# Kernel optimization log

Measured on AMD Instinct MI355X. Metric: run time of the kernel, lower is better.

Reference implementation:

```python
import jax, jax.numpy as jnp
import numpy as np

B, M, E, H, TOPK = 1024, 10000, 8, 512, 2


def setup_inputs() -> dict:
    key = jax.random.key(0)
    ks = jax.random.split(key, 6)
    s_in = 1.0 / np.sqrt(M)
    s_h = 1.0 / np.sqrt(H)
    x = jax.random.normal(ks[0], (B, M), dtype=jnp.float32)
    # Expert params, torch Linear layout stacked over experts
    W1 = jax.random.uniform(ks[1], (E, H, M), jnp.float32, -s_in, s_in)
    b1 = jax.random.uniform(ks[2], (E, H), jnp.float32, -s_in, s_in)
    W2 = jax.random.uniform(ks[3], (E, M, H), jnp.float32, -s_h, s_h)
    b2 = jax.random.uniform(ks[4], (E, M), jnp.float32, -s_h, s_h)
    Wr = jax.random.uniform(ks[5], (E, M), jnp.float32, -s_in, s_in)  # router, no bias
    return {"x": x, "W1": W1, "b1": b1, "W2": W2, "b2": b2, "Wr": Wr}


def reference(x, W1, b1, W2, b2, Wr):
    # Router: logits [B, E], sparse top-k softmax weights scattered to dense [B, E]
    logits = jnp.einsum('bm,em->be', x, Wr)
    topk_vals, topk_idx = jax.lax.top_k(logits, TOPK)
    probs = jax.nn.softmax(topk_vals, axis=-1)
    rw = jnp.zeros_like(logits).at[jnp.arange(B)[:, None], topk_idx].set(probs)
    # Dense all-expert MLP (faithful to original: every expert runs on every token)
    h = jax.nn.relu(jnp.einsum('bm,ehm->beh', x, W1) + b1)      # [B, E, H]
    eo = jnp.einsum('beh,emh->bem', h, W2) + b2                  # [B, E, M]
    # Masked weighted combine
    out = jnp.sum(rw[:, :, None] * eo, axis=1)                   # [B, M]
    return out
```

## Files before the change

### kernel.cpp

```cpp
#include <hip/hip_runtime.h>
#include <hip/hip_bf16.h>


#define B_TOK 1024
#define M_DIM 10000
#define E_NUM 8
#define H_DIM 512
#define NSTEP 313
#define SPAD1 316

typedef __attribute__((ext_vector_type(4))) float fx4;
typedef __attribute__((ext_vector_type(8))) short sx8;
typedef __attribute__((ext_vector_type(4))) short sx4;

__device__ __forceinline__ short f2bf(float f) {
  union { __hip_bfloat16 h; short s; } u;
  u.h = __float2bfloat16(f);
  return u.s;
}

__device__ __forceinline__ sx8 pack8(fx4 a, fx4 b) {
  sx8 r;
  r[0] = f2bf(a[0]); r[1] = f2bf(a[1]); r[2] = f2bf(a[2]); r[3] = f2bf(a[3]);
  r[4] = f2bf(b[0]); r[5] = f2bf(b[1]); r[6] = f2bf(b[2]); r[7] = f2bf(b[3]);
  return r;
}

__device__ __forceinline__ void gload16(const short* g, short* l) {
  __builtin_amdgcn_global_load_lds(
      (const __attribute__((address_space(1))) void*)g,
      (__attribute__((address_space(3))) void*)l, 16, 0, 0);
}

__global__ void k_zero(int* cnt, int* cnt2, int* zpad) {
  if (threadIdx.x < E_NUM) cnt[threadIdx.x] = 0;
  if (threadIdx.x < 2 * E_NUM) cnt2[threadIdx.x] = 0;
  if (threadIdx.x < 16) zpad[threadIdx.x] = 0;
}

__global__ __launch_bounds__(256) void k_router(
    const float* __restrict__ x, const float* __restrict__ Wr,
    int* __restrict__ cnt, int* __restrict__ cnt2,
    int* __restrict__ tokAll, int* __restrict__ qlist2, float* __restrict__ wlist2,
    short* __restrict__ xb)
{
  int b = blockIdx.x, t = threadIdx.x;
  const float* xr = x + (size_t)b * M_DIM;
  short* xbr = xb + (size_t)b * M_DIM;
  double acc[E_NUM];
#pragma unroll
  for (int e = 0; e < E_NUM; e++) acc[e] = 0.0;
  for (int m = t; m < M_DIM; m += 256) {
    float xv = xr[m];
    xbr[m] = f2bf(xv);
#pragma unroll
    for (int e = 0; e < E_NUM; e++)
      acc[e] += (double)xv * (double)Wr[e * M_DIM + m];
  }
#pragma unroll
  for (int e = 0; e < E_NUM; e++) {
#pragma unroll
    for (int off = 32; off > 0; off >>= 1)
      acc[e] += __shfl_xor(acc[e], off);
  }
  __shared__ double part[4][E_NUM];
  int wave = t >> 6;
  if ((t & 63) == 0) {
    for (int e = 0; e < E_NUM; e++) part[wave][e] = acc[e];
  }
  __syncthreads();
  if (t == 0) {
    double lg[E_NUM];
    for (int e = 0; e < E_NUM; e++)
      lg[e] = part[0][e] + part[1][e] + part[2][e] + part[3][e];
    int i0 = 0;
    for (int e = 1; e < E_NUM; e++) if (lg[e] > lg[i0]) i0 = e;
    int i1 = (i0 == 0) ? 1 : 0;
    for (int e = 0; e < E_NUM; e++) if (e != i0 && lg[e] > lg[i1]) i1 = e;
    double ex = exp(lg[i1] - lg[i0]);
    float p0 = (float)(1.0 / (1.0 + ex));
    float p1 = (float)(ex / (1.0 + ex));
    int q0 = atomicAdd(&cnt[i0], 1);
    tokAll[i0 * B_TOK + q0] = b;
    int j0 = atomicAdd(&cnt2[i0 * 2 + 0], 1);
    qlist2[(i0 * 2 + 0) * B_TOK + j0] = q0;
    wlist2[(i0 * 2 + 0) * B_TOK + j0] = p0;
    int q1 = atomicAdd(&cnt[i1], 1);
    tokAll[i1 * B_TOK + q1] = b;
    int j1 = atomicAdd(&cnt2[i1 * 2 + 1], 1);
    qlist2[(i1 * 2 + 1) * B_TOK + j1] = q1;
    wlist2[(i1 * 2 + 1) * B_TOK + j1] = p1;
  }
}

__global__ __launch_bounds__(256) void k_cvt1T(
    const float* __restrict__ W1, short* __restrict__ WbT)
{
  int e = blockIdx.z, nt = blockIdx.y, sc = blockIdx.x;
  __shared__ short tile[128][136];
  int t = threadIdx.x;
  int row = t >> 1, ch = (t & 1) * 64;
  const float* src = W1 + ((size_t)e * H_DIM + nt * 128 + row) * M_DIM;
  int c0 = sc * 128 + ch;
  if (c0 + 64 <= M_DIM) {
#pragma unroll
    for (int j = 0; j < 8; j++) {
      fx4 a = *(const fx4*)(src + c0 + j * 8);
      fx4 b = *(const fx4*)(src + c0 + j * 8 + 4);
      *(sx8*)&tile[row][ch + j * 8] = pack8(a, b);
    }
  } else {
    for (int j = 0; j < 64; j++) {
      int c = c0 + j;
      tile[row][ch + j] = (c < M_DIM) ? f2bf(src[c]) : (short)0;
    }
  }
  __syncthreads();
  size_t base = ((size_t)(e * 4 + nt) * SPAD1 + sc * 4) * 4096;
  int c0w = (t & 1) * 16;
  int r = t >> 1;
#pragma unroll
  for (int sp = 0; sp < 4; sp++) {
    sx8 v0 = *(sx8*)&tile[r][sp * 32 + c0w];
    sx8 v1 = *(sx8*)&tile[r][sp * 32 + c0w + 8];
    short* dst = WbT + base + (size_t)sp * 4096 + t * 16;
    *(sx8*)(dst) = v0;
    *(sx8*)(dst + 8) = v1;
  }
}

__global__ __launch_bounds__(256) void k_cvt2T(
    const float* __restrict__ W2, short* __restrict__ WbT)
{
  int e = blockIdx.z, mt = blockIdx.y, sc = blockIdx.x;
  __shared__ short tile[128][136];
  int t = threadIdx.x;
  int row = t >> 1, ch = (t & 1) * 64;
  int grow = mt * 128 + row;
  int c0 = sc * 128 + ch;
  if (grow < M_DIM) {
    const float* src = W2 + ((size_t)e * M_DIM + grow) * H_DIM;
#pragma unroll
    for (int j = 0; j < 8; j++) {
      fx4 a = *(const fx4*)(src + c0 + j * 8);
      fx4 b = *(const fx4*)(src + c0 + j * 8 + 4);
      *(sx8*)&tile[row][ch + j * 8] = pack8(a, b);
    }
  } else {
    sx8 z = {0, 0, 0, 0, 0, 0, 0, 0};
#pragma unroll
    for (int j = 0; j < 8; j++) *(sx8*)&tile[row][ch + j * 8] = z;
  }
  __syncthreads();
  size_t base = ((size_t)(e * 79 + mt) * 16 + sc * 4) * 4096;
  int c0w = (t & 1) * 16;
  int r = t >> 1;
#pragma unroll
  for (int sp = 0; sp < 4; sp++) {
    sx8 v0 = *(sx8*)&tile[r][sp * 32 + c0w];
    sx8 v1 = *(sx8*)&tile[r][sp * 32 + c0w + 8];
    short* dst = WbT + base + (size_t)sp * 4096 + t * 16;
    *(sx8*)(dst) = v0;
    *(sx8*)(dst + 8) = v1;
  }
}

#define M_MFMA2(cb)                                                         \
  do {                                                                      \
    sx8 af[4], bfr[4];                                                      \
    _Pragma("unroll")                                                       \
    for (int m_ = 0; m_ < 4; m_++)                                          \
      af[m_] = *(const sx8*)(LA[cb] + (wr * 64 + m_ * 16 + lrow) * 32 + khalf * 8); \
    _Pragma("unroll")                                                       \
    for (int n_ = 0; n_ < 4; n_++)                                          \
      bfr[n_] = *(const sx8*)(LB[cb] + (wc * 64 + n_ * 16 + lrow) * 32 + khalf * 8); \
    __builtin_amdgcn_s_setprio(1);                                          \
    _Pragma("unroll")                                                       \
    for (int m_ = 0; m_ < 4; m_++)                                          \
      _Pragma("unroll")                                                     \
      for (int n_ = 0; n_ < 4; n_++)                                        \
        acc[m_][n_] = __builtin_amdgcn_mfma_f32_16x16x32_bf16(af[m_], bfr[n_], acc[m_][n_], 0, 0, 0); \
    __builtin_amdgcn_s_setprio(0);                                          \
  } while (0)

__global__ __launch_bounds__(256) void k_mlp1g(
    const short* __restrict__ xb, const short* __restrict__ WbT,
    const int* __restrict__ cnt, const int* __restrict__ tokAll,
    float* __restrict__ partials, const short* __restrict__ zpad, int CH)
{
  int e = blockIdx.z;
  int tt = blockIdx.y >> 2, nt = blockIdx.y & 3;
  int kc = blockIdx.x;

  __shared__ int sh_ne, sh_eoff;
  __shared__ __align__(16) short LA[2][4096];
  __shared__ __align__(16) short LB[2][4096];
  __shared__ int toks[128];

  int t = threadIdx.x;
  if (t == 0) {
    int off = 0;
    for (int k = 0; k < e; k++) off += cnt[k];
    sh_eoff = off; sh_ne = cnt[e];
  }
  __syncthreads();
  int ne = sh_ne, eoff = sh_eoff, row0 = tt * 128;
  if (row0 >= ne) return;
  int nvalid = min(128, ne - row0);
  if (t < 128) toks[t] = tokAll[e * B_TOK + row0 + min(t, nvalid - 1)];
  __syncthreads();

  int lane = t & 63, wave = t >> 6;
  int srA = wave * 32 + (lane >> 2);
  int scol = (lane & 3) * 8;
  const short* ap0 = xb + (size_t)toks[srA] * M_DIM + scol;
  const short* ap1 = xb + (size_t)toks[srA + 16] * M_DIM + scol;
  int ldA0 = (wave * 32) * 32, ldA1 = (wave * 32 + 16) * 32;
  const short* bbase = WbT + ((size_t)(e * 4 + nt) * SPAD1) * 4096;
  int bo = wave * 1024;
  int blane = bo + lane * 8;

  int wr = wave >> 1, wc = wave & 1;
  int lrow = lane & 15, khalf = lane >> 4;

  fx4 z4 = {0.f, 0.f, 0.f, 0.f};
  fx4 acc[4][4];
#pragma unroll
  for (int m = 0; m < 4; m++)
#pragma unroll
    for (int n = 0; n < 4; n++) acc[m][n] = z4;

  int s0 = kc * CH, s1 = min(s0 + CH, NSTEP);

#define STAGE1(buf, sN)                                        \
  do {                                                         \
    int ko_ = (sN) * 32;                                       \
    bool ok_ = (ko_ + scol + 8 <= M_DIM);                      \
    gload16(ok_ ? (ap0 + ko_) : zpad, LA[buf] + ldA0);         \
    gload16(ok_ ? (ap1 + ko_) : zpad, LA[buf] + ldA1);         \
    const short* bs_ = bbase + (size_t)(sN) * 4096 + blane;    \
    gload16(bs_, LB[buf] + bo);                                \
    gload16(bs_ + 512, LB[buf] + bo + 512);                    \
  } while (0)

  STAGE1(0, s0);
  __syncthreads();

  int c = 0;
  for (int s = s0; s < s1; s++) {
    if (s + 1 < s1) STAGE1(c ^ 1, s + 1);
    M_MFMA2(c);
    __syncthreads();
    c ^= 1;
  }

#pragma unroll
  for (int m = 0; m < 4; m++)
#pragma unroll
    for (int n = 0; n < 4; n++) {
      int colg = nt * 128 + wc * 64 + n * 16 + lrow;
#pragma unroll
      for (int r = 0; r < 4; r++) {
        int rl = wr * 64 + m * 16 + khalf * 4 + r;
        if (rl < nvalid) {
          int grow = eoff + row0 + rl;
          partials[((size_t)kc * 2048 + grow) * H_DIM + colg] = acc[m][n][r];
        }
      }
    }
#undef STAGE1
}

__global__ __launch_bounds__(256) void k_hreduce(
    const float* __restrict__ partials, const float* __restrict__ b1,
    const int* __restrict__ cnt, short* __restrict__ hbuf, int KC)
{
  __shared__ int sc[E_NUM];
  int t = threadIdx.x;
  if (t < E_NUM) sc[t] = cnt[t];
  __syncthreads();
  int i = (blockIdx.x * 256 + t) * 4;
  int slot = i >> 9;
  int e = 0, off = 0;
  for (int k = 0; k < E_NUM - 1; k++) {
    if (slot >= off + sc[k]) { off += sc[k]; e++; } else break;
  }
  fx4 v = *(const fx4*)(partials + i);
  for (int kc = 1; kc < KC; kc++)
    v += *(const fx4*)(partials + (size_t)kc * 2048 * H_DIM + i);
  fx4 bv = *(const fx4*)(b1 + e * H_DIM + (i & (H_DIM - 1)));
  sx4 o;
#pragma unroll
  for (int j = 0; j < 4; j++) o[j] = f2bf(fmaxf(v[j] + bv[j], 0.f));
  *(sx4*)(hbuf + i) = o;
}

__global__ __launch_bounds__(256) void k_mlp2g(
    const short* __restrict__ hbuf, const short* __restrict__ WbT,
    const float* __restrict__ b2, const int* __restrict__ cnt,
    const int* __restrict__ cnt2, const int* __restrict__ tokAll,
    const int* __restrict__ qlist2, const float* __restrict__ wlist2,
    float* __restrict__ out, int ord)
{
  int e = blockIdx.z, mt = blockIdx.x, tt = blockIdx.y;

  __shared__ int sh_ne2, sh_eoff;
  __shared__ __align__(16) short LA[2][4096];
  __shared__ __align__(16) short LB[2][4096];
  __shared__ int sl[128];
  __shared__ int tok2[128];
  __shared__ float wts[128];

  int t = threadIdx.x;
  if (t == 0) {
    int off = 0;
    for (int k = 0; k < e; k++) off += cnt[k];
    sh_eoff = off; sh_ne2 = cnt2[e * 2 + ord];
  }
  __syncthreads();
  int ne2 = sh_ne2, eoff = sh_eoff, row0 = tt * 128;
  if (row0 >= ne2) return;
  int nvalid = min(128, ne2 - row0);

  if (t < 128) {
    int j = row0 + min(t, nvalid - 1);
    int q = qlist2[(e * 2 + ord) * B_TOK + j];
    sl[t] = eoff + q;
    tok2[t] = tokAll[e * B_TOK + q];
    wts[t] = (t < nvalid) ? wlist2[(e * 2 + ord) * B_TOK + j] : 0.f;
  }
  __syncthreads();

  int lane = t & 63, wave = t >> 6;
  int srA = wave * 32 + (lane >> 2);
  int scol = (lane & 3) * 8;
  const short* ap0 = hbuf + (size_t)sl[srA] * H_DIM + scol;
  const short* ap1 = hbuf + (size_t)sl[srA + 16] * H_DIM + scol;
  int ldA0 = (wave * 32) * 32, ldA1 = (wave * 32 + 16) * 32;
  const short* bbase = WbT + ((size_t)(e * 79 + mt) * 16) * 4096;
  int bo = wave * 1024;
  int blane = bo + lane * 8;

  int wr = wave >> 1, wc = wave & 1;
  int lrow = lane & 15, khalf = lane >> 4;

  fx4 z4 = {0.f, 0.f, 0.f, 0.f};
  fx4 acc[4][4];
#pragma unroll
  for (int m = 0; m < 4; m++)
#pragma unroll
    for (int n = 0; n < 4; n++) acc[m][n] = z4;

#define STAGE2(buf, sN)                                        \
  do {                                                         \
    int ko_ = (sN) * 32;                                       \
    gload16(ap0 + ko_, LA[buf] + ldA0);                        \
    gload16(ap1 + ko_, LA[buf] + ldA1);                        \
    const short* bs_ = bbase + (size_t)(sN) * 4096 + blane;    \
    gload16(bs_, LB[buf] + bo);                                \
    gload16(bs_ + 512, LB[buf] + bo + 512);                    \
  } while (0)

  STAGE2(0, 0);
  __syncthreads();

  int c = 0;
  for (int s = 0; s < 16; s++) {
    if (s + 1 < 16) STAGE2(c ^ 1, s + 1);
    M_MFMA2(c);
    __syncthreads();
    c ^= 1;
  }

#pragma unroll
  for (int m = 0; m < 4; m++)
#pragma unroll
    for (int n = 0; n < 4; n++) {
      int colg = mt * 128 + wc * 64 + n * 16 + lrow;
      if (colg < M_DIM) {
        float b2v = b2[(size_t)e * M_DIM + colg];
#pragma unroll
        for (int r = 0; r < 4; r++) {
          int rl = wr * 64 + m * 16 + khalf * 4 + r;
          if (rl < nvalid) {
            float v = wts[rl] * (acc[m][n][r] + b2v);
            float* dst = out + (size_t)tok2[rl] * M_DIM + colg;
            if (ord == 0) *dst = v;
            else *dst += v;
          }
        }
      }
    }
#undef STAGE2
}

extern "C" void kernel_launch(void* const* d_in, const int* in_sizes, int n_in,
                              void* d_out, int out_size, void* d_ws, size_t ws_size,
                              hipStream_t stream) {
  const float* x  = (const float*)d_in[0];
  const float* W1 = (const float*)d_in[1];
  const float* b1 = (const float*)d_in[2];
  const float* W2 = (const float*)d_in[3];
  const float* b2 = (const float*)d_in[4];
  const float* Wr = (const float*)d_in[5];
  float* out = (float*)d_out;

  int KC = (ws_size >= 139200000ULL) ? 8 : 5;
  int CH = (NSTEP + KC - 1) / KC;

  char* p = (char*)d_ws;
  float* partials = (float*)p;        p += (size_t)KC * 2048 * H_DIM * 4;
  short* hbuf     = (short*)p;        p += (size_t)2048 * H_DIM * 2;
  int*   cnt      = (int*)p;          p += 64;
  int*   cnt2     = (int*)p;          p += 64;
  int*   tokAll   = (int*)p;          p += E_NUM * B_TOK * 4;
  int*   qlist2   = (int*)p;          p += 2 * E_NUM * B_TOK * 4;
  float* wlist2   = (float*)p;        p += 2 * E_NUM * B_TOK * 4;
  int*   zpad     = (int*)p;          p += 64;
  short* xb       = (short*)p;        p += (size_t)B_TOK * M_DIM * 2;
  short* WbT      = (short*)p;

  k_zero<<<1, 64, 0, stream>>>(cnt, cnt2, zpad);
  k_router<<<B_TOK, 256, 0, stream>>>(x, Wr, cnt, cnt2, tokAll, qlist2, wlist2, xb);
  k_cvt1T<<<dim3(79, 4, E_NUM), 256, 0, stream>>>(W1, WbT);
  k_mlp1g<<<dim3(KC, 32, E_NUM), 256, 0, stream>>>(xb, WbT, cnt, tokAll, partials,
                                                   (const short*)zpad, CH);
  k_hreduce<<<1024, 256, 0, stream>>>(partials, b1, cnt, hbuf, KC);
  k_cvt2T<<<dim3(4, 79, E_NUM), 256, 0, stream>>>(W2, WbT);
  k_mlp2g<<<dim3(79, 8, E_NUM), 256, 0, stream>>>(hbuf, WbT, b2, cnt, cnt2, tokAll,
                                                  qlist2, wlist2, out, 0);
  k_mlp2g<<<dim3(79, 8, E_NUM), 256, 0, stream>>>(hbuf, WbT, b2, cnt, cnt2, tokAll,
                                                  qlist2, wlist2, out, 1);
}
```

Baseline: 364.1 us.

## Retile second expert GEMM to 64-token tiles and split K further

The second-layer expert GEMM kernel now uses 64-row token tiles with 128 threads (two waves, each covering 64 output columns) instead of 128-row tiles with 256 threads, and the launch grid doubles along the token axis. Because each expert/order slot holds only about 128 tokens, the old grid left most token tiles idle, so this change is meant to raise the number of active blocks. When the workspace is large enough, the first GEMM's K-split also goes from 8 to 16 chunks, and W2 gets its own buffer so its conversion can be issued before the first GEMM. The cost is less reuse of each B tile per load, more partial-sum memory traffic in the reduction, and extra workspace.

```diff
diff --git a/kernel.cpp b/kernel.cpp
--- a/kernel.cpp
+++ b/kernel.cpp
@@ -295,7 +295,7 @@
   *(sx4*)(hbuf + i) = o;
 }
 
-__global__ __launch_bounds__(256) void k_mlp2g(
+__global__ __launch_bounds__(128) void k_mlp2g2(
     const short* __restrict__ hbuf, const short* __restrict__ WbT,
     const float* __restrict__ b2, const int* __restrict__ cnt,
     const int* __restrict__ cnt2, const int* __restrict__ tokAll,
@@ -305,11 +305,11 @@
   int e = blockIdx.z, mt = blockIdx.x, tt = blockIdx.y;
 
   __shared__ int sh_ne2, sh_eoff;
-  __shared__ __align__(16) short LA[2][4096];
+  __shared__ __align__(16) short LA[2][2048];
   __shared__ __align__(16) short LB[2][4096];
-  __shared__ int sl[128];
-  __shared__ int tok2[128];
-  __shared__ float wts[128];
+  __shared__ int sl[64];
+  __shared__ int tok2[64];
+  __shared__ float wts[64];
 
   int t = threadIdx.x;
   if (t == 0) {
@@ -318,11 +318,11 @@
     sh_eoff = off; sh_ne2 = cnt2[e * 2 + ord];
   }
   __syncthreads();
-  int ne2 = sh_ne2, eoff = sh_eoff, row0 = tt * 128;
+  int ne2 = sh_ne2, eoff = sh_eoff, row0 = tt * 64;
   if (row0 >= ne2) return;
-  int nvalid = min(128, ne2 - row0);
-
-  if (t < 128) {
+  int nvalid = min(64, ne2 - row0);
+
+  if (t < 64) {
     int j = row0 + min(t, nvalid - 1);
     int q = qlist2[(e * 2 + ord) * B_TOK + j];
     sl[t] = eoff + q;
@@ -332,16 +332,16 @@
   __syncthreads();
 
   int lane = t & 63, wave = t >> 6;
+  int scol = (lane & 3) * 8;
   int srA = wave * 32 + (lane >> 2);
-  int scol = (lane & 3) * 8;
   const short* ap0 = hbuf + (size_t)sl[srA] * H_DIM + scol;
   const short* ap1 = hbuf + (size_t)sl[srA + 16] * H_DIM + scol;
   int ldA0 = (wave * 32) * 32, ldA1 = (wave * 32 + 16) * 32;
   const short* bbase = WbT + ((size_t)(e * 79 + mt) * 16) * 4096;
-  int bo = wave * 1024;
+  int bo = wave * 2048;
   int blane = bo + lane * 8;
 
-  int wr = wave >> 1, wc = wave & 1;
+  int wc = wave;
   int lrow = lane & 15, khalf = lane >> 4;
 
   fx4 z4 = {0.f, 0.f, 0.f, 0.f};
@@ -359,6 +359,8 @@
     const short* bs_ = bbase + (size_t)(sN) * 4096 + blane;    \
     gload16(bs_, LB[buf] + bo);                                \
     gload16(bs_ + 512, LB[buf] + bo + 512);                    \
+    gload16(bs_ + 1024, LB[buf] + bo + 1024);                  \
+    gload16(bs_ + 1536, LB[buf] + bo + 1536);                  \
   } while (0)
 
   STAGE2(0, 0);
@@ -367,7 +369,22 @@
   int c = 0;
   for (int s = 0; s < 16; s++) {
     if (s + 1 < 16) STAGE2(c ^ 1, s + 1);
-    M_MFMA2(c);
+    {
+      sx8 af[4], bfr[4];
+#pragma unroll
+      for (int m_ = 0; m_ < 4; m_++)
+        af[m_] = *(const sx8*)(LA[c] + (m_ * 16 + lrow) * 32 + khalf * 8);
+#pragma unroll
+      for (int n_ = 0; n_ < 4; n_++)
+        bfr[n_] = *(const sx8*)(LB[c] + (wc * 64 + n_ * 16 + lrow) * 32 + khalf * 8);
+      __builtin_amdgcn_s_setprio(1);
+#pragma unroll
+      for (int m_ = 0; m_ < 4; m_++)
+#pragma unroll
+        for (int n_ = 0; n_ < 4; n_++)
+          acc[m_][n_] = __builtin_amdgcn_mfma_f32_16x16x32_bf16(af[m_], bfr[n_], acc[m_][n_], 0, 0, 0);
+      __builtin_amdgcn_s_setprio(0);
+    }
     __syncthreads();
     c ^= 1;
   }
@@ -381,7 +398,7 @@
         float b2v = b2[(size_t)e * M_DIM + colg];
 #pragma unroll
         for (int r = 0; r < 4; r++) {
-          int rl = wr * 64 + m * 16 + khalf * 4 + r;
+          int rl = m * 16 + khalf * 4 + r;
           if (rl < nvalid) {
             float v = wts[rl] * (acc[m][n][r] + b2v);
             float* dst = out + (size_t)tok2[rl] * M_DIM + colg;
@@ -405,8 +422,10 @@
   const float* Wr = (const float*)d_in[5];
   float* out = (float*)d_out;
 
-  int KC = (ws_size >= 139200000ULL) ? 8 : 5;
+  int big = (ws_size >= 280000000ULL);
+  int KC = big ? 16 : 8;
   int CH = (NSTEP + KC - 1) / KC;
+  const size_t WBT_BYTES = (size_t)E_NUM * 4 * SPAD1 * 4096 * 2;
 
   char* p = (char*)d_ws;
   float* partials = (float*)p;        p += (size_t)KC * 2048 * H_DIM * 4;
@@ -418,17 +437,19 @@
   float* wlist2   = (float*)p;        p += 2 * E_NUM * B_TOK * 4;
   int*   zpad     = (int*)p;          p += 64;
   short* xb       = (short*)p;        p += (size_t)B_TOK * M_DIM * 2;
-  short* WbT      = (short*)p;
+  short* WbT1     = (short*)p;        p += WBT_BYTES;
+  short* WbT2     = big ? (short*)p : WbT1;
 
   k_zero<<<1, 64, 0, stream>>>(cnt, cnt2, zpad);
   k_router<<<B_TOK, 256, 0, stream>>>(x, Wr, cnt, cnt2, tokAll, qlist2, wlist2, xb);
-  k_cvt1T<<<dim3(79, 4, E_NUM), 256, 0, stream>>>(W1, WbT);
-  k_mlp1g<<<dim3(KC, 32, E_NUM), 256, 0, stream>>>(xb, WbT, cnt, tokAll, partials,
+  k_cvt1T<<<dim3(79, 4, E_NUM), 256, 0, stream>>>(W1, WbT1);
+  if (big) k_cvt2T<<<dim3(4, 79, E_NUM), 256, 0, stream>>>(W2, WbT2);
+  k_mlp1g<<<dim3(KC, 32, E_NUM), 256, 0, stream>>>(xb, WbT1, cnt, tokAll, partials,
                                                    (const short*)zpad, CH);
   k_hreduce<<<1024, 256, 0, stream>>>(partials, b1, cnt, hbuf, KC);
-  k_cvt2T<<<dim3(4, 79, E_NUM), 256, 0, stream>>>(W2, WbT);
-  k_mlp2g<<<dim3(79, 8, E_NUM), 256, 0, stream>>>(hbuf, WbT, b2, cnt, cnt2, tokAll,
-                                                  qlist2, wlist2, out, 0);
-  k_mlp2g<<<dim3(79, 8, E_NUM), 256, 0, stream>>>(hbuf, WbT, b2, cnt, cnt2, tokAll,
-                                                  qlist2, wlist2, out, 1);
-}
+  if (!big) k_cvt2T<<<dim3(4, 79, E_NUM), 256, 0, stream>>>(W2, WbT2);
+  k_mlp2g2<<<dim3(79, 16, E_NUM), 128, 0, stream>>>(hbuf, WbT2, b2, cnt, cnt2, tokAll,
+                                                    qlist2, wlist2, out, 0);
+  k_mlp2g2<<<dim3(79, 16, E_NUM), 128, 0, stream>>>(hbuf, WbT2, b2, cnt, cnt2, tokAll,
+                                                    qlist2, wlist2, out, 1);
+}
```

Result: slower. 381.1 us (+4.7%).
